# Kernel tuning notes

Measured on AMD Instinct MI355X. Metric: run time of the kernel, lower is better.

The kernel has to match this reference:

```python
import jax, jax.numpy as jnp
import numpy as np
from jax import lax

EPS = 1e-5
SLOPE = 0.01  # default leaky_relu negative slope

def _conv1d(x, w):
    # x: [B, Cin, L], w: [Cout, Cin, K]; padding=1 (same for K=3)
    return lax.conv_general_dilated(x, w, window_strides=(1,), padding=[(1, 1)],
                                    dimension_numbers=('NCH', 'OIH', 'NCH'))

def _bn_train(x, gamma, beta, axes):
    # training-mode BatchNorm: batch stats over `axes`, biased variance
    mean = jnp.mean(x, axis=axes, keepdims=True)
    var = jnp.mean(jnp.square(x - mean), axis=axes, keepdims=True)
    shape = [1] * x.ndim
    shape[1] = x.shape[1]
    g = gamma.reshape(shape); b = beta.reshape(shape)
    return (x - mean) * g / jnp.sqrt(var + EPS) + b

def setup_inputs() -> dict:
    key = jax.random.key(0)
    ks = jax.random.split(key, 6)
    d, d2, out_dim = 64, 128, 128
    bs, T, N = 16, 32, 256
    s = 0.05
    return {
        'x': jax.random.normal(ks[0], (bs, T, N, d), jnp.float32),
        'conv1_w': jax.random.normal(ks[1], (d2, d, 3), jnp.float32) * s,
        'bn1_g': jnp.ones((d2,), jnp.float32), 'bn1_b': jnp.zeros((d2,), jnp.float32),
        'conv2_w': jax.random.normal(ks[2], (d2, d2, 3), jnp.float32) * s,
        'bn2_g': jnp.ones((d2,), jnp.float32), 'bn2_b': jnp.zeros((d2,), jnp.float32),
        'map_w': jax.random.normal(ks[3], (d2, d2), jnp.float32) * s,
        'map_b': jnp.zeros((d2,), jnp.float32),
        'theta_w': jax.random.normal(ks[4], (out_dim, d2), jnp.float32) * s,
        'theta_b': jnp.zeros((out_dim,), jnp.float32),
        'bnS_g': jnp.ones((out_dim,), jnp.float32), 'bnS_b': jnp.zeros((out_dim,), jnp.float32),
    }

def reference(x, conv1_w, bn1_g, bn1_b, conv2_w, bn2_g, bn2_b,
              map_w, map_b, theta_w, theta_b, bnS_g, bnS_b):
    bs, T, N, d = x.shape
    d2 = 2 * d
    # ---- Temporal 1D CNN over time, per node ----
    tem = jnp.transpose(x, (0, 2, 1, 3)).reshape(bs * N, T, d)      # [BN, T, d]
    h = jnp.transpose(tem, (0, 2, 1))                               # [BN, d, T]
    h = jax.nn.relu(_bn_train(_conv1d(h, conv1_w), bn1_g, bn1_b, (0, 2)))
    h = jax.nn.relu(_bn_train(_conv1d(h, conv2_w), bn2_g, bn2_b, (0, 2)))  # [BN, 2d, T]
    # faithful raw reshape (mixes channel/time layout exactly like the torch code)
    tem_out = h.reshape(bs, N, T, d2)
    spa = jnp.transpose(tem_out, (0, 2, 1, 3)).reshape(bs * T, N, d2)  # [B', N, 2d]
    # ---- Dot-product graph construction ----
    mapped = jnp.einsum('bnd,ed->bne', spa, map_w) + map_b            # Linear(2d,2d)
    adj = jnp.einsum('bnd,bmd->bnm', mapped, mapped)                  # [B', N, N]
    eye = jnp.eye(N, dtype=adj.dtype)
    adj = jax.nn.leaky_relu(adj - eye * 1e8, SLOPE)
    adj = jax.nn.softmax(adj, axis=-1) + eye
    # ---- MPNN (k=1): theta(A @ X), BN over channels, leaky_relu ----
    agg = jnp.einsum('bnm,bmd->bnd', adj, spa)                        # bmm(A, X)
    out = jnp.einsum('bnd,od->bno', agg, theta_w) + theta_b           # [B', N, out]
    out = jnp.transpose(out, (0, 2, 1))                               # [B', out, N]
    out = _bn_train(out, bnS_g, bnS_b, (0, 2))
    out = jnp.transpose(out, (0, 2, 1))
    return jax.nn.leaky_relu(out, SLOPE)
```

## Files before the change

kernel.cpp:

```cpp
#include <hip/hip_runtime.h>

#define SLOPE 0.01f
#define EPSB 1e-5f
#define INV_CNT (1.0f/131072.0f)

typedef unsigned short u16;
typedef unsigned int u32;
typedef __attribute__((ext_vector_type(8))) short s16x8;
typedef __attribute__((ext_vector_type(4))) float f4;

__device__ float g_stats[3][2][128];
__device__ float g_sb[3][2][128];
__device__ float g_part[2048][256];
__device__ int   g_cnt[3];
__device__ u16 g_w1h[3][128][64];
__device__ u16 g_w1l[3][128][64];
__device__ u16 g_w2h[3][128][128];
__device__ u16 g_w2l[3][128][128];
__device__ u16 g_wmh[128][128];
__device__ u16 g_wml[128][128];
__device__ u16 g_wqh[128][128];
__device__ u16 g_wql[128][128];
__device__ u16 g_sT[16777216];

__device__ __forceinline__ float lrelu(float x){ return x > 0.f ? x : SLOPE*x; }
__device__ __forceinline__ u16 f2b(float f){
  u32 u = __float_as_uint(f);
  return (u16)((u + 0x7fffu + ((u >> 16) & 1u)) >> 16);
}
__device__ __forceinline__ float b2f(u16 h){ return __uint_as_float(((u32)h) << 16); }
__device__ __forceinline__ u32 pk(float a, float b){ return (u32)f2b(a) | ((u32)f2b(b) << 16); }

__global__ void k_prepw(const float* __restrict__ w1, const float* __restrict__ w2,
                        const float* __restrict__ mapw, const float* __restrict__ thw){
  int idx = blockIdx.x*256 + threadIdx.x;
  if (idx < 768) ((float*)g_stats)[idx] = 0.f;
  if (idx < 3) g_cnt[idx] = 0;
  if (idx < 24576){
    int kk = idx >> 13, r = idx & 8191, co = r >> 6, ci = r & 63;
    float v = w1[co*192 + ci*3 + kk];
    u16 h = f2b(v);
    g_w1h[kk][co][ci] = h; g_w1l[kk][co][ci] = f2b(v - b2f(h));
  } else if (idx < 73728){
    int j = idx - 24576;
    int kk = j >> 14, r = j & 16383, co = r >> 7, ci = r & 127;
    float v = w2[co*384 + ci*3 + kk];
    u16 h = f2b(v);
    g_w2h[kk][co][ci] = h; g_w2l[kk][co][ci] = f2b(v - b2f(h));
  } else if (idx < 90112){
    int j = idx - 73728;
    float v = mapw[j];
    u16 h = f2b(v);
    ((u16*)g_wmh)[j] = h; ((u16*)g_wml)[j] = f2b(v - b2f(h));
  } else if (idx < 106496){
    int j = idx - 90112;
    float v = thw[j];
    u16 h = f2b(v);
    ((u16*)g_wqh)[j] = h; ((u16*)g_wql)[j] = f2b(v - b2f(h));
  }
}

__global__ void k_reduce(const float* __restrict__ g, const float* __restrict__ bta, int which){
  const float* base = &g_part[blockIdx.x*128][0];
  int j = threadIdx.x;
  float s = 0.f;
  #pragma unroll 4
  for (int r = 0; r < 128; ++r) s += base[r*256 + j];
  atomicAdd(&((float*)g_stats)[which*256 + j], s);
  __threadfence();
  __shared__ int lastf;
  __syncthreads();
  if (threadIdx.x == 0) lastf = (atomicAdd(&g_cnt[which], 1) == 15) ? 1 : 0;
  __syncthreads();
  if (lastf){
    __threadfence();
    if (j < 128){
      float sm = atomicAdd(&g_stats[which][0][j], 0.f);
      float sq = atomicAdd(&g_stats[which][1][j], 0.f);
      float mean = sm * INV_CNT;
      float var  = sq * INV_CNT - mean*mean;
      float sc = g[j] * rsqrtf(var + EPSB);
      g_sb[which][0][j] = sc;
      g_sb[which][1][j] = bta[j] - mean*sc;
    }
  }
}

__global__ __launch_bounds__(256, 4) void k_conv1(const float* __restrict__ x, float* __restrict__ y1f){
  __shared__ __align__(16) u16 a0h[2][34][72];
  __shared__ __align__(16) u16 a0l[2][34][72];
  const int bid = blockIdx.x;
  const int bn0 = bid*2;
  const int b = bn0 >> 8, n = bn0 & 255;
  const int tid = threadIdx.x;
  const int w = tid >> 6, l = tid & 63, quad = l >> 4, lm = l & 15;
  f4 acc[2][4];
  #pragma unroll
  for (int i = 0; i < 2; ++i)
    #pragma unroll
    for (int j = 0; j < 4; ++j) acc[i][j] = (f4)0.f;

  {
    int nn = tid >> 7, rem = tid & 127, t = rem >> 2, ci0 = (rem & 3)*16;
    const float* px = x + ((b*32 + t)*256 + n + nn)*64 + ci0;
    u16 hh[16], ll[16];
    #pragma unroll
    for (int j = 0; j < 4; ++j){
      float4 v = *(const float4*)(px + 4*j);
      float vv[4] = {v.x, v.y, v.z, v.w};
      #pragma unroll
      for (int e = 0; e < 4; ++e){
        u16 h = f2b(vv[e]);
        hh[4*j+e] = h; ll[4*j+e] = f2b(vv[e] - b2f(h));
      }
    }
    *(uint4*)&a0h[nn][t+1][ci0]   = *(uint4*)&hh[0];
    *(uint4*)&a0h[nn][t+1][ci0+8] = *(uint4*)&hh[8];
    *(uint4*)&a0l[nn][t+1][ci0]   = *(uint4*)&ll[0];
    *(uint4*)&a0l[nn][t+1][ci0+8] = *(uint4*)&ll[8];
  }
  for (int u = tid; u < 288; u += 256){
    int a = u / 144, rr = u % 144, r = rr / 36, cw = rr % 36;
    u32* base = a ? (u32*)&a0l[r>>1][(r&1)*33][0] : (u32*)&a0h[r>>1][(r&1)*33][0];
    base[cw] = 0u;
  }
  __syncthreads();

  for (int kk = 0; kk < 3; ++kk){
    #pragma unroll
    for (int s = 0; s < 2; ++s){
      int ci0 = s*32 + quad*8;
      s16x8 wh[2], wl[2], bh[4], bl[4];
      #pragma unroll
      for (int i = 0; i < 2; ++i){
        wh[i] = *(const s16x8*)&g_w1h[kk][(2*w+i)*16 + lm][ci0];
        wl[i] = *(const s16x8*)&g_w1l[kk][(2*w+i)*16 + lm][ci0];
      }
      #pragma unroll
      for (int nt = 0; nt < 4; ++nt){
        bh[nt] = *(s16x8*)&a0h[nt>>1][(nt&1)*16 + lm + kk][ci0];
        bl[nt] = *(s16x8*)&a0l[nt>>1][(nt&1)*16 + lm + kk][ci0];
      }
      #pragma unroll
      for (int i = 0; i < 2; ++i)
        #pragma unroll
        for (int nt = 0; nt < 4; ++nt){
          acc[i][nt] = __builtin_amdgcn_mfma_f32_16x16x32_bf16(wh[i], bh[nt], acc[i][nt], 0, 0, 0);
          acc[i][nt] = __builtin_amdgcn_mfma_f32_16x16x32_bf16(wh[i], bl[nt], acc[i][nt], 0, 0, 0);
          acc[i][nt] = __builtin_amdgcn_mfma_f32_16x16x32_bf16(wl[i], bh[nt], acc[i][nt], 0, 0, 0);
        }
    }
  }
  #pragma unroll
  for (int i = 0; i < 2; ++i){
    int co0 = (2*w+i)*16 + quad*4;
    float s0=0,s1=0,s2=0,s3=0,q0=0,q1=0,q2=0,q3=0;
    #pragma unroll
    for (int nt = 0; nt < 4; ++nt){
      f4 a = acc[i][nt];
      int nn = nt >> 1, t = (nt & 1)*16 + lm;
      *(f4*)&y1f[((bn0+nn)*32 + t)*128 + co0] = a;
      s0+=a.x; s1+=a.y; s2+=a.z; s3+=a.w;
      q0+=a.x*a.x; q1+=a.y*a.y; q2+=a.z*a.z; q3+=a.w*a.w;
    }
    #pragma unroll
    for (int m = 1; m < 16; m <<= 1){
      s0+=__shfl_xor(s0,m); s1+=__shfl_xor(s1,m); s2+=__shfl_xor(s2,m); s3+=__shfl_xor(s3,m);
      q0+=__shfl_xor(q0,m); q1+=__shfl_xor(q1,m); q2+=__shfl_xor(q2,m); q3+=__shfl_xor(q3,m);
    }
    if (lm == 0){
      f4 sv = {s0,s1,s2,s3}, qv = {q0,q1,q2,q3};
      *(f4*)&g_part[bid][co0]       = sv;
      *(f4*)&g_part[bid][128 + co0] = qv;
    }
  }
}

__global__ __launch_bounds__(256, 4) void k_conv2(const float* __restrict__ y1f, u16* __restrict__ spa){
  __shared__ __align__(16) u16 a1s[2][34][136];
  const int bid = blockIdx.x;
  const int bn0 = bid*2;
  const int b = bn0 >> 8, n = bn0 & 255;
  const int tid = threadIdx.x;
  const int w = tid >> 6, l = tid & 63, quad = l >> 4, lm = l & 15;
  f4 acc2[4][2];
  #pragma unroll
  for (int mt = 0; mt < 4; ++mt)
    #pragma unroll
    for (int i = 0; i < 2; ++i) acc2[mt][i] = (f4)0.f;

  {
    int nn = tid >> 7, rem = tid & 127, t = rem >> 2, ci0 = (rem & 3)*32;
    const float* py = y1f + ((bn0+nn)*32 + t)*128;
    #pragma unroll
    for (int j = 0; j < 4; ++j){
      float4 v1 = *(const float4*)(py + ci0 + 8*j);
      float4 v2 = *(const float4*)(py + ci0 + 8*j + 4);
      float vv[8] = {v1.x, v1.y, v1.z, v1.w, v2.x, v2.y, v2.z, v2.w};
      u16 oo[8];
      #pragma unroll
      for (int e = 0; e < 8; ++e){
        int ci = ci0 + 8*j + e;
        oo[e] = f2b(fmaxf(fmaf(vv[e], g_sb[0][0][ci], g_sb[0][1][ci]), 0.f));
      }
      *(uint4*)&a1s[nn][t+1][ci0 + 8*j] = *(uint4*)&oo[0];
    }
  }
  for (int u = tid; u < 272; u += 256){
    int r = u/68, cw = u%68;
    ((u32*)&a1s[r>>1][(r&1)*33][0])[cw] = 0u;
  }
  __syncthreads();

  for (int kk = 0; kk < 3; ++kk){
    #pragma unroll
    for (int s = 0; s < 4; ++s){
      int ci0 = s*32 + quad*8;
      s16x8 ax[4], bwh[2], bwl[2];
      #pragma unroll
      for (int i = 0; i < 2; ++i){
        bwh[i] = *(const s16x8*)&g_w2h[kk][(2*w+i)*16 + lm][ci0];
        bwl[i] = *(const s16x8*)&g_w2l[kk][(2*w+i)*16 + lm][ci0];
      }
      #pragma unroll
      for (int mt = 0; mt < 4; ++mt) ax[mt] = *(s16x8*)&a1s[mt>>1][(mt&1)*16 + lm + kk][ci0];
      #pragma unroll
      for (int mt = 0; mt < 4; ++mt)
        #pragma unroll
        for (int i = 0; i < 2; ++i){
          acc2[mt][i] = __builtin_amdgcn_mfma_f32_16x16x32_bf16(ax[mt], bwh[i], acc2[mt][i], 0, 0, 0);
          acc2[mt][i] = __builtin_amdgcn_mfma_f32_16x16x32_bf16(ax[mt], bwl[i], acc2[mt][i], 0, 0, 0);
        }
    }
  }
  #pragma unroll
  for (int i = 0; i < 2; ++i){
    int co = (2*w+i)*16 + lm;
    float s = 0.f, q = 0.f;
    #pragma unroll
    for (int mt = 0; mt < 4; ++mt){
      f4 a = acc2[mt][i];
      int off0 = co*32 + (mt&1)*16 + quad*4;
      int tp = off0 >> 7, cp = off0 & 127;
      int row = (b*32 + tp)*256 + (n + (mt>>1));
      uint2 p; p.x = pk(a.x, a.y); p.y = pk(a.z, a.w);
      *(uint2*)&spa[row*128 + cp] = p;
      s += a.x + a.y + a.z + a.w;
      q += a.x*a.x + a.y*a.y + a.z*a.z + a.w*a.w;
    }
    s += __shfl_xor(s, 16); s += __shfl_xor(s, 32);
    q += __shfl_xor(q, 16); q += __shfl_xor(q, 32);
    if (l < 16){
      g_part[bid][co]       = s;
      g_part[bid][128 + co] = q;
    }
  }
}

__global__ __launch_bounds__(256, 4) void k_gemm128b(const u16* A,
                                                     u16* spaw,
                                                     const float* __restrict__ bvec,
                                                     void* __restrict__ outv,
                                                     int wsel, int do_stats){
  __shared__ __align__(16) u16 As[64][136];
  const u16* Wh = wsel ? &g_wqh[0][0] : &g_wmh[0][0];
  const u16* Wl = wsel ? &g_wql[0][0] : &g_wml[0][0];
  const int bid = blockIdx.x;
  const int rowbase = bid * 64;
  const int tid = threadIdx.x;
  const int w = tid >> 6, l = tid & 63, quad = l >> 4, lm = l & 15;
  f4 acc[2][4];
  #pragma unroll
  for (int i = 0; i < 2; ++i)
    #pragma unroll
    for (int rt = 0; rt < 4; ++rt) acc[i][rt] = (f4)0.f;

  { int r = tid >> 2, c0 = (tid & 3)*32;
    int row = rowbase + r;
    if (wsel == 0){
      int c = ((row >> 8) & 31)*4 + (tid & 3);
      float sc = g_sb[1][0][c], bi = g_sb[1][1][c];
      int mrel = row & 63;
      u16* st = g_sT + (((row >> 6) * 128) << 6);
      #pragma unroll
      for (int j = 0; j < 4; ++j){
        uint4 v = *(const uint4*)&A[row*128 + c0 + 8*j];
        u32 vv[4] = {v.x, v.y, v.z, v.w};
        u16 oo[8];
        #pragma unroll
        for (int e = 0; e < 4; ++e){
          oo[2*e]   = f2b(fmaxf(fmaf(b2f((u16)(vv[e] & 0xffff)), sc, bi), 0.f));
          oo[2*e+1] = f2b(fmaxf(fmaf(b2f((u16)(vv[e] >> 16)),    sc, bi), 0.f));
        }
        uint4 ov = *(uint4*)&oo[0];
        *(uint4*)&As[r][c0 + 8*j] = ov;
        *(uint4*)&spaw[row*128 + c0 + 8*j] = ov;
        #pragma unroll
        for (int e = 0; e < 8; ++e)
          st[(c0 + 8*j + e)*64 + mrel] = oo[e];
      }
    } else {
      #pragma unroll
      for (int j = 0; j < 4; ++j)
        *(uint4*)&As[r][c0 + 8*j] = *(const uint4*)&A[row*128 + c0 + 8*j];
    }
  }
  __syncthreads();

  #pragma unroll
  for (int s = 0; s < 4; ++s){
    int k0 = s*32 + quad*8;
    s16x8 awh[2], awl[2], ba[4];
    #pragma unroll
    for (int i = 0; i < 2; ++i){
      awh[i] = *(const s16x8*)&Wh[((2*w+i)*16 + lm)*128 + k0];
      awl[i] = *(const s16x8*)&Wl[((2*w+i)*16 + lm)*128 + k0];
    }
    #pragma unroll
    for (int rt = 0; rt < 4; ++rt) ba[rt] = *(s16x8*)&As[rt*16 + lm][k0];
    #pragma unroll
    for (int i = 0; i < 2; ++i)
      #pragma unroll
      for (int rt = 0; rt < 4; ++rt){
        acc[i][rt] = __builtin_amdgcn_mfma_f32_16x16x32_bf16(awh[i], ba[rt], acc[i][rt], 0, 0, 0);
        acc[i][rt] = __builtin_amdgcn_mfma_f32_16x16x32_bf16(awl[i], ba[rt], acc[i][rt], 0, 0, 0);
      }
  }
  #pragma unroll
  for (int i = 0; i < 2; ++i){
    int e0 = (2*w+i)*16 + quad*4;
    f4 bv = *(const f4*)&bvec[e0];
    if (wsel == 0){
      u16* mh = (u16*)outv;
      u16* ml = mh + 16777216;
      int dc = e0 >> 5, ec = e0 & 31;
      #pragma unroll
      for (int rt = 0; rt < 4; ++rt){
        int row = rowbase + rt*16 + lm;
        int bp = row >> 8, m = row & 255;
        f4 o = acc[i][rt] + bv;
        float fv[4] = {o.x, o.y, o.z, o.w};
        u16 hh[4], ll[4];
        #pragma unroll
        for (int e = 0; e < 4; ++e){
          u16 h = f2b(fv[e]);
          hh[e] = h; ll[e] = f2b(fv[e] - b2f(h));
        }
        int off = ((bp*4 + dc)*256 + m)*32 + ec;
        *(uint2*)&mh[off] = *(uint2*)&hh[0];
        *(uint2*)&ml[off] = *(uint2*)&ll[0];
      }
    } else {
      float* outp = (float*)outv;
      f4 sv = (f4)0.f, qv = (f4)0.f;
      #pragma unroll
      for (int rt = 0; rt < 4; ++rt){
        int row = rowbase + rt*16 + lm;
        f4 o = acc[i][rt] + bv;
        *(f4*)&outp[row*128 + e0] = o;
        sv += o; qv += o*o;
      }
      if (do_stats){
        #pragma unroll
        for (int m = 1; m < 16; m <<= 1){
          sv.x+=__shfl_xor(sv.x,m); sv.y+=__shfl_xor(sv.y,m); sv.z+=__shfl_xor(sv.z,m); sv.w+=__shfl_xor(sv.w,m);
          qv.x+=__shfl_xor(qv.x,m); qv.y+=__shfl_xor(qv.y,m); qv.z+=__shfl_xor(qv.z,m); qv.w+=__shfl_xor(qv.w,m);
        }
        if (lm == 0){
          *(f4*)&g_part[bid][e0]       = sv;
          *(f4*)&g_part[bid][128 + e0] = qv;
        }
      }
    }
  }
}

__global__ __launch_bounds__(256) void k_adjagg(const u16* __restrict__ mh,
                                                const u16* __restrict__ ml,
                                                const u16* __restrict__ spa,
                                                u16* __restrict__ agg){
  __shared__ __align__(16) char smem[52224];
  u16 (*mbh)[40]   = (u16(*)[40])(smem);
  u16 (*mbl)[40]   = (u16(*)[40])(smem + 20480);
  u16 (*Ps)[264]   = (u16(*)[264])(smem);
  u16 (*spasT)[72] = (u16(*)[72])(smem + 33792);
  const int rb = blockIdx.x;
  const int vb = (rb & 7)*256 + (rb >> 3);
  const int bp = vb >> 2;
  const int nt = vb & 3;
  const int tid = threadIdx.x;
  const int w = tid >> 6, l = tid & 63, quad = l >> 4, lm = l & 15;

  f4 sacc[16];
  #pragma unroll
  for (int ct = 0; ct < 16; ++ct) sacc[ct] = (f4)0.f;

  for (int dc = 0; dc < 4; ++dc){
    __syncthreads();
    {
      const u16* srch = mh + ((bp*4 + dc) << 13);
      const u16* srcl = ml + ((bp*4 + dc) << 13);
      int m0 = tid >> 2, seg = (tid & 3)*8;
      #pragma unroll
      for (int r = 0; r < 4; ++r){
        int m = m0 + r*64;
        *(uint4*)&mbh[m][seg] = *(const uint4*)&srch[m*32 + seg];
        *(uint4*)&mbl[m][seg] = *(const uint4*)&srcl[m*32 + seg];
      }
    }
    __syncthreads();
    s16x8 amh = *(s16x8*)&mbh[nt*64 + w*16 + lm][quad*8];
    s16x8 aml = *(s16x8*)&mbl[nt*64 + w*16 + lm][quad*8];
    #pragma unroll
    for (int ct = 0; ct < 16; ++ct){
      s16x8 bmh = *(s16x8*)&mbh[ct*16 + lm][quad*8];
      s16x8 bml = *(s16x8*)&mbl[ct*16 + lm][quad*8];
      sacc[ct] = __builtin_amdgcn_mfma_f32_16x16x32_bf16(amh, bmh, sacc[ct], 0, 0, 0);
      sacc[ct] = __builtin_amdgcn_mfma_f32_16x16x32_bf16(amh, bml, sacc[ct], 0, 0, 0);
      sacc[ct] = __builtin_amdgcn_mfma_f32_16x16x32_bf16(aml, bmh, sacc[ct], 0, 0, 0);
    }
  }
  __syncthreads();

  #pragma unroll
  for (int r = 0; r < 4; ++r){
    int rowg = nt*64 + w*16 + quad*4 + r;
    float v[16]; float mx = -3.0e38f;
    #pragma unroll
    for (int ct = 0; ct < 16; ++ct){
      float t = sacc[ct][r];
      if (ct*16 + lm == rowg) t -= 1e8f;
      t = lrelu(t);
      v[ct] = t; mx = fmaxf(mx, t);
    }
    #pragma unroll
    for (int m = 1; m < 16; m <<= 1) mx = fmaxf(mx, __shfl_xor(mx, m));
    float sum = 0.f;
    #pragma unroll
    for (int ct = 0; ct < 16; ++ct){ float e = __expf(v[ct] - mx); v[ct] = e; sum += e; }
    #pragma unroll
    for (int m = 1; m < 16; m <<= 1) sum += __shfl_xor(sum, m);
    float inv = 1.0f / sum;
    #pragma unroll
    for (int ct = 0; ct < 16; ++ct)
      Ps[w*16 + quad*4 + r][ct*16 + lm] = f2b(v[ct] * inv);
  }

  f4 acc2[2][4];
  #pragma unroll
  for (int i = 0; i < 2; ++i)
    #pragma unroll
    for (int rt = 0; rt < 4; ++rt) acc2[i][rt] = (f4)0.f;

  for (int mc2 = 0; mc2 < 4; ++mc2){
    __syncthreads();
    {
      const u16* src = g_sT + (((bp*4 + mc2)*128) << 6) + (tid >> 1)*64 + (tid & 1)*32;
      u16* dst = &spasT[tid >> 1][(tid & 1)*32];
      *(uint4*)(dst)      = *(const uint4*)(src);
      *(uint4*)(dst + 8)  = *(const uint4*)(src + 8);
      *(uint4*)(dst + 16) = *(const uint4*)(src + 16);
      *(uint4*)(dst + 24) = *(const uint4*)(src + 24);
    }
    __syncthreads();
    #pragma unroll
    for (int ks = 0; ks < 2; ++ks){
      int m0 = ks*32 + quad*8;
      s16x8 afs[2], bfp[4];
      #pragma unroll
      for (int i = 0; i < 2; ++i) afs[i] = *(s16x8*)&spasT[(2*w+i)*16 + lm][m0];
      #pragma unroll
      for (int rt = 0; rt < 4; ++rt) bfp[rt] = *(s16x8*)&Ps[rt*16 + lm][mc2*64 + m0];
      #pragma unroll
      for (int i = 0; i < 2; ++i)
        #pragma unroll
        for (int rt = 0; rt < 4; ++rt)
          acc2[i][rt] = __builtin_amdgcn_mfma_f32_16x16x32_bf16(afs[i], bfp[rt], acc2[i][rt], 0, 0, 0);
    }
  }
  #pragma unroll
  for (int i = 0; i < 2; ++i){
    int d0 = (2*w+i)*16 + quad*4;
    #pragma unroll
    for (int rt = 0; rt < 4; ++rt){
      int grow = bp*256 + nt*64 + rt*16 + lm;
      uint2 sp = *(const uint2*)&spa[grow*128 + d0];
      f4 a = acc2[i][rt];
      a.x += b2f((u16)(sp.x & 0xffff)); a.y += b2f((u16)(sp.x >> 16));
      a.z += b2f((u16)(sp.y & 0xffff)); a.w += b2f((u16)(sp.y >> 16));
      uint2 p; p.x = pk(a.x, a.y); p.y = pk(a.z, a.w);
      *(uint2*)&agg[grow*128 + d0] = p;
    }
  }
}

__global__ void k_bnout(float* __restrict__ outp){
  int idx = blockIdx.x*256 + threadIdx.x;
  int flat = idx*4;
  int o = flat & 127;
  float4 v = *(const float4*)(outp + flat);
  v.x = lrelu(fmaf(v.x, g_sb[2][0][o+0], g_sb[2][1][o+0]));
  v.y = lrelu(fmaf(v.y, g_sb[2][0][o+1], g_sb[2][1][o+1]));
  v.z = lrelu(fmaf(v.z, g_sb[2][0][o+2], g_sb[2][1][o+2]));
  v.w = lrelu(fmaf(v.w, g_sb[2][0][o+3], g_sb[2][1][o+3]));
  *(float4*)(outp + flat) = v;
}

extern "C" void kernel_launch(void* const* d_in, const int* in_sizes, int n_in,
                              void* d_out, int out_size, void* d_ws, size_t ws_size,
                              hipStream_t stream) {
  const float* x    = (const float*)d_in[0];
  const float* w1   = (const float*)d_in[1];
  const float* bn1g = (const float*)d_in[2];
  const float* bn1b = (const float*)d_in[3];
  const float* w2   = (const float*)d_in[4];
  const float* bn2g = (const float*)d_in[5];
  const float* bn2b = (const float*)d_in[6];
  const float* mapw = (const float*)d_in[7];
  const float* mapb = (const float*)d_in[8];
  const float* thw  = (const float*)d_in[9];
  const float* thb  = (const float*)d_in[10];
  const float* bnSg = (const float*)d_in[11];
  const float* bnSb = (const float*)d_in[12];
  float* outp = (float*)d_out;

  u16* spa = (u16*)d_ws;
  u16* agg = spa + 16777216;

  float* y1f = (float*)d_out;
  u16* mh    = (u16*)d_out;

  k_prepw<<<416, 256, 0, stream>>>(w1, w2, mapw, thw);
  k_conv1<<<2048, 256, 0, stream>>>(x, y1f);
  k_reduce<<<16, 256, 0, stream>>>(bn1g, bn1b, 0);
  k_conv2<<<2048, 256, 0, stream>>>(y1f, spa);
  k_reduce<<<16, 256, 0, stream>>>(bn2g, bn2b, 1);
  k_gemm128b<<<2048, 256, 0, stream>>>(spa, spa, mapb, (void*)mh, 0, 0);
  k_adjagg<<<2048, 256, 0, stream>>>(mh, mh + 16777216, spa, agg);
  k_gemm128b<<<2048, 256, 0, stream>>>(agg, agg, thb, (void*)outp, 1, 1);
  k_reduce<<<16, 256, 0, stream>>>(bnSg, bnSb, 2);
  k_bnout<<<16384, 256, 0, stream>>>(outp);
}
```

Before: 407.5 us.

## Fuse theta GEMM, output BatchNorm and leaky ReLU via grid-wide barrier

```diff
diff --git a/kernel.cpp b/kernel.cpp
--- a/kernel.cpp
+++ b/kernel.cpp
@@ -257,14 +257,13 @@
   }
 }
 
-__global__ __launch_bounds__(256, 4) void k_gemm128b(const u16* A,
-                                                     u16* spaw,
-                                                     const float* __restrict__ bvec,
-                                                     void* __restrict__ outv,
-                                                     int wsel, int do_stats){
+__global__ __launch_bounds__(256, 4) void k_gemm0(const u16* A,
+                                                  u16* spaw,
+                                                  const float* __restrict__ bvec,
+                                                  u16* __restrict__ mh){
   __shared__ __align__(16) u16 As[64][136];
-  const u16* Wh = wsel ? &g_wqh[0][0] : &g_wmh[0][0];
-  const u16* Wl = wsel ? &g_wql[0][0] : &g_wml[0][0];
+  const u16* Wh = &g_wmh[0][0];
+  const u16* Wl = &g_wml[0][0];
   const int bid = blockIdx.x;
   const int rowbase = bid * 64;
   const int tid = threadIdx.x;
@@ -277,32 +276,26 @@
 
   { int r = tid >> 2, c0 = (tid & 3)*32;
     int row = rowbase + r;
-    if (wsel == 0){
-      int c = ((row >> 8) & 31)*4 + (tid & 3);
-      float sc = g_sb[1][0][c], bi = g_sb[1][1][c];
-      int mrel = row & 63;
-      u16* st = g_sT + (((row >> 6) * 128) << 6);
-      #pragma unroll
-      for (int j = 0; j < 4; ++j){
-        uint4 v = *(const uint4*)&A[row*128 + c0 + 8*j];
-        u32 vv[4] = {v.x, v.y, v.z, v.w};
-        u16 oo[8];
-        #pragma unroll
-        for (int e = 0; e < 4; ++e){
-          oo[2*e]   = f2b(fmaxf(fmaf(b2f((u16)(vv[e] & 0xffff)), sc, bi), 0.f));
-          oo[2*e+1] = f2b(fmaxf(fmaf(b2f((u16)(vv[e] >> 16)),    sc, bi), 0.f));
-        }
-        uint4 ov = *(uint4*)&oo[0];
-        *(uint4*)&As[r][c0 + 8*j] = ov;
-        *(uint4*)&spaw[row*128 + c0 + 8*j] = ov;
-        #pragma unroll
-        for (int e = 0; e < 8; ++e)
-          st[(c0 + 8*j + e)*64 + mrel] = oo[e];
-      }
-    } else {
-      #pragma unroll
-      for (int j = 0; j < 4; ++j)
-        *(uint4*)&As[r][c0 + 8*j] = *(const uint4*)&A[row*128 + c0 + 8*j];
+    int c = ((row >> 8) & 31)*4 + (tid & 3);
+    float sc = g_sb[1][0][c], bi = g_sb[1][1][c];
+    int mrel = row & 63;
+    u16* st = g_sT + (((row >> 6) * 128) << 6);
+    #pragma unroll
+    for (int j = 0; j < 4; ++j){
+      uint4 v = *(const uint4*)&A[row*128 + c0 + 8*j];
+      u32 vv[4] = {v.x, v.y, v.z, v.w};
+      u16 oo[8];
+      #pragma unroll
+      for (int e = 0; e < 4; ++e){
+        oo[2*e]   = f2b(fmaxf(fmaf(b2f((u16)(vv[e] & 0xffff)), sc, bi), 0.f));
+        oo[2*e+1] = f2b(fmaxf(fmaf(b2f((u16)(vv[e] >> 16)),    sc, bi), 0.f));
+      }
+      uint4 ov = *(uint4*)&oo[0];
+      *(uint4*)&As[r][c0 + 8*j] = ov;
+      *(uint4*)&spaw[row*128 + c0 + 8*j] = ov;
+      #pragma unroll
+      for (int e = 0; e < 8; ++e)
+        st[(c0 + 8*j + e)*64 + mrel] = oo[e];
     }
   }
   __syncthreads();
@@ -330,47 +323,23 @@
   for (int i = 0; i < 2; ++i){
     int e0 = (2*w+i)*16 + quad*4;
     f4 bv = *(const f4*)&bvec[e0];
-    if (wsel == 0){
-      u16* mh = (u16*)outv;
-      u16* ml = mh + 16777216;
-      int dc = e0 >> 5, ec = e0 & 31;
-      #pragma unroll
-      for (int rt = 0; rt < 4; ++rt){
-        int row = rowbase + rt*16 + lm;
-        int bp = row >> 8, m = row & 255;
-        f4 o = acc[i][rt] + bv;
-        float fv[4] = {o.x, o.y, o.z, o.w};
-        u16 hh[4], ll[4];
-        #pragma unroll
-        for (int e = 0; e < 4; ++e){
-          u16 h = f2b(fv[e]);
-          hh[e] = h; ll[e] = f2b(fv[e] - b2f(h));
-        }
-        int off = ((bp*4 + dc)*256 + m)*32 + ec;
-        *(uint2*)&mh[off] = *(uint2*)&hh[0];
-        *(uint2*)&ml[off] = *(uint2*)&ll[0];
-      }
-    } else {
-      float* outp = (float*)outv;
-      f4 sv = (f4)0.f, qv = (f4)0.f;
-      #pragma unroll
-      for (int rt = 0; rt < 4; ++rt){
-        int row = rowbase + rt*16 + lm;
-        f4 o = acc[i][rt] + bv;
-        *(f4*)&outp[row*128 + e0] = o;
-        sv += o; qv += o*o;
-      }
-      if (do_stats){
-        #pragma unroll
-        for (int m = 1; m < 16; m <<= 1){
-          sv.x+=__shfl_xor(sv.x,m); sv.y+=__shfl_xor(sv.y,m); sv.z+=__shfl_xor(sv.z,m); sv.w+=__shfl_xor(sv.w,m);
-          qv.x+=__shfl_xor(qv.x,m); qv.y+=__shfl_xor(qv.y,m); qv.z+=__shfl_xor(qv.z,m); qv.w+=__shfl_xor(qv.w,m);
-        }
-        if (lm == 0){
-          *(f4*)&g_part[bid][e0]       = sv;
-          *(f4*)&g_part[bid][128 + e0] = qv;
-        }
-      }
+    u16* ml = mh + 16777216;
+    int dc = e0 >> 5, ec = e0 & 31;
+    #pragma unroll
+    for (int rt = 0; rt < 4; ++rt){
+      int row = rowbase + rt*16 + lm;
+      int bp = row >> 8, m = row & 255;
+      f4 o = acc[i][rt] + bv;
+      float fv[4] = {o.x, o.y, o.z, o.w};
+      u16 hh[4], ll[4];
+      #pragma unroll
+      for (int e = 0; e < 4; ++e){
+        u16 h = f2b(fv[e]);
+        hh[e] = h; ll[e] = f2b(fv[e] - b2f(h));
+      }
+      int off = ((bp*4 + dc)*256 + m)*32 + ec;
+      *(uint2*)&mh[off] = *(uint2*)&hh[0];
+      *(uint2*)&ml[off] = *(uint2*)&ll[0];
     }
   }
 }
@@ -494,16 +463,136 @@
   }
 }
 
-__global__ void k_bnout(float* __restrict__ outp){
-  int idx = blockIdx.x*256 + threadIdx.x;
-  int flat = idx*4;
-  int o = flat & 127;
-  float4 v = *(const float4*)(outp + flat);
-  v.x = lrelu(fmaf(v.x, g_sb[2][0][o+0], g_sb[2][1][o+0]));
-  v.y = lrelu(fmaf(v.y, g_sb[2][0][o+1], g_sb[2][1][o+1]));
-  v.z = lrelu(fmaf(v.z, g_sb[2][0][o+2], g_sb[2][1][o+2]));
-  v.w = lrelu(fmaf(v.w, g_sb[2][0][o+3], g_sb[2][1][o+3]));
-  *(float4*)(outp + flat) = v;
+__global__ __launch_bounds__(256, 4) void k_gemm1c(const u16* __restrict__ A,
+                                                   const float* __restrict__ bvec,
+                                                   const float* __restrict__ g,
+                                                   const float* __restrict__ bta,
+                                                   float* __restrict__ outp){
+  __shared__ __align__(16) u16 As[64][136];
+  __shared__ __align__(16) u16 stash[64][132];
+  __shared__ float sbS[2][128];
+  const u16* Wh = &g_wqh[0][0];
+  const u16* Wl = &g_wql[0][0];
+  const int bid = blockIdx.x;
+  const int tid = threadIdx.x;
+  const int w = tid >> 6, l = tid & 63, quad = l >> 4, lm = l & 15;
+
+  f4 o0[2][4], o1[2][4];
+  f4 sv[2] = {(f4)0.f, (f4)0.f}, qv[2] = {(f4)0.f, (f4)0.f};
+
+  #pragma unroll
+  for (int ti = 0; ti < 2; ++ti){
+    const int rowbase = bid*128 + ti*64;
+    f4 acc[2][4];
+    #pragma unroll
+    for (int i = 0; i < 2; ++i)
+      #pragma unroll
+      for (int rt = 0; rt < 4; ++rt) acc[i][rt] = (f4)0.f;
+
+    if (ti) __syncthreads();
+    { int r = tid >> 2, c0 = (tid & 3)*32;
+      #pragma unroll
+      for (int j = 0; j < 4; ++j)
+        *(uint4*)&As[r][c0 + 8*j] = *(const uint4*)&A[(rowbase + r)*128 + c0 + 8*j];
+    }
+    __syncthreads();
+
+    #pragma unroll
+    for (int s = 0; s < 4; ++s){
+      int k0 = s*32 + quad*8;
+      s16x8 awh[2], awl[2], ba[4];
+      #pragma unroll
+      for (int i = 0; i < 2; ++i){
+        awh[i] = *(const s16x8*)&Wh[((2*w+i)*16 + lm)*128 + k0];
+        awl[i] = *(const s16x8*)&Wl[((2*w+i)*16 + lm)*128 + k0];
+      }
+      #pragma unroll
+      for (int rt = 0; rt < 4; ++rt) ba[rt] = *(s16x8*)&As[rt*16 + lm][k0];
+      #pragma unroll
+      for (int i = 0; i < 2; ++i)
+        #pragma unroll
+        for (int rt = 0; rt < 4; ++rt){
+          acc[i][rt] = __builtin_amdgcn_mfma_f32_16x16x32_bf16(awh[i], ba[rt], acc[i][rt], 0, 0, 0);
+          acc[i][rt] = __builtin_amdgcn_mfma_f32_16x16x32_bf16(awl[i], ba[rt], acc[i][rt], 0, 0, 0);
+        }
+    }
+    #pragma unroll
+    for (int i = 0; i < 2; ++i){
+      int e0 = (2*w+i)*16 + quad*4;
+      f4 bv = *(const f4*)&bvec[e0];
+      #pragma unroll
+      for (int rt = 0; rt < 4; ++rt){
+        f4 o = acc[i][rt] + bv;
+        if (ti == 0){
+          o0[i][rt] = o;
+          uint2 p; p.x = pk(o.x, o.y); p.y = pk(o.z, o.w);
+          *(uint2*)&stash[rt*16 + lm][e0] = p;
+        } else {
+          o1[i][rt] = o;
+        }
+        sv[i] += o; qv[i] += o*o;
+      }
+    }
+  }
+  (void)o0;
+
+  #pragma unroll
+  for (int i = 0; i < 2; ++i){
+    #pragma unroll
+    for (int m = 1; m < 16; m <<= 1){
+      sv[i].x+=__shfl_xor(sv[i].x,m); sv[i].y+=__shfl_xor(sv[i].y,m);
+      sv[i].z+=__shfl_xor(sv[i].z,m); sv[i].w+=__shfl_xor(sv[i].w,m);
+      qv[i].x+=__shfl_xor(qv[i].x,m); qv[i].y+=__shfl_xor(qv[i].y,m);
+      qv[i].z+=__shfl_xor(qv[i].z,m); qv[i].w+=__shfl_xor(qv[i].w,m);
+    }
+    if (lm == 0){
+      int e0 = (2*w+i)*16 + quad*4;
+      atomicAdd(&g_stats[2][0][e0+0], sv[i].x); atomicAdd(&g_stats[2][0][e0+1], sv[i].y);
+      atomicAdd(&g_stats[2][0][e0+2], sv[i].z); atomicAdd(&g_stats[2][0][e0+3], sv[i].w);
+      atomicAdd(&g_stats[2][1][e0+0], qv[i].x); atomicAdd(&g_stats[2][1][e0+1], qv[i].y);
+      atomicAdd(&g_stats[2][1][e0+2], qv[i].z); atomicAdd(&g_stats[2][1][e0+3], qv[i].w);
+    }
+  }
+  __threadfence();
+  __syncthreads();
+  if (tid == 0){
+    atomicAdd(&g_cnt[2], 1);
+    while (atomicAdd(&g_cnt[2], 0) < 1024) __builtin_amdgcn_s_sleep(16);
+  }
+  __syncthreads();
+  __threadfence();
+  if (tid < 128){
+    float sm = atomicAdd(&g_stats[2][0][tid], 0.f);
+    float sq = atomicAdd(&g_stats[2][1][tid], 0.f);
+    float mean = sm * INV_CNT;
+    float var  = sq * INV_CNT - mean*mean;
+    float sc = g[tid] * rsqrtf(var + EPSB);
+    sbS[0][tid] = sc;
+    sbS[1][tid] = bta[tid] - mean*sc;
+  }
+  __syncthreads();
+  #pragma unroll
+  for (int i = 0; i < 2; ++i){
+    int e0 = (2*w+i)*16 + quad*4;
+    f4 sc = *(const f4*)&sbS[0][e0];
+    f4 bi = *(const f4*)&sbS[1][e0];
+    #pragma unroll
+    for (int rt = 0; rt < 4; ++rt){
+      uint2 p = *(const uint2*)&stash[rt*16 + lm][e0];
+      f4 t0;
+      t0.x = b2f((u16)(p.x & 0xffff)); t0.y = b2f((u16)(p.x >> 16));
+      t0.z = b2f((u16)(p.y & 0xffff)); t0.w = b2f((u16)(p.y >> 16));
+      f4 r0;
+      r0.x = lrelu(fmaf(t0.x, sc.x, bi.x)); r0.y = lrelu(fmaf(t0.y, sc.y, bi.y));
+      r0.z = lrelu(fmaf(t0.z, sc.z, bi.z)); r0.w = lrelu(fmaf(t0.w, sc.w, bi.w));
+      *(f4*)&outp[(bid*128 + rt*16 + lm)*128 + e0] = r0;
+      f4 o = o1[i][rt];
+      f4 r1;
+      r1.x = lrelu(fmaf(o.x, sc.x, bi.x)); r1.y = lrelu(fmaf(o.y, sc.y, bi.y));
+      r1.z = lrelu(fmaf(o.z, sc.z, bi.z)); r1.w = lrelu(fmaf(o.w, sc.w, bi.w));
+      *(f4*)&outp[(bid*128 + 64 + rt*16 + lm)*128 + e0] = r1;
+    }
+  }
 }
 
 extern "C" void kernel_launch(void* const* d_in, const int* in_sizes, int n_in,
@@ -535,9 +624,7 @@
   k_reduce<<<16, 256, 0, stream>>>(bn1g, bn1b, 0);
   k_conv2<<<2048, 256, 0, stream>>>(y1f, spa);
   k_reduce<<<16, 256, 0, stream>>>(bn2g, bn2b, 1);
-  k_gemm128b<<<2048, 256, 0, stream>>>(spa, spa, mapb, (void*)mh, 0, 0);
+  k_gemm0<<<2048, 256, 0, stream>>>(spa, spa, mapb, mh);
   k_adjagg<<<2048, 256, 0, stream>>>(mh, mh + 16777216, spa, agg);
-  k_gemm128b<<<2048, 256, 0, stream>>>(agg, agg, thb, (void*)outp, 1, 1);
-  k_reduce<<<16, 256, 0, stream>>>(bnSg, bnSb, 2);
-  k_bnout<<<16384, 256, 0, stream>>>(outp);
-}
+  k_gemm1c<<<1024, 256, 0, stream>>>(agg, thb, bnSg, bnSb, outp);
+}
```

Measured after the change: 692.3 us. +69.9%, slower.

## Store intermediates in bf16 and drop the transposed spa copy

Applied to the files above, without the earlier changes.

```diff
diff --git a/kernel.cpp b/kernel.cpp
--- a/kernel.cpp
+++ b/kernel.cpp
@@ -21,7 +21,6 @@
 __device__ u16 g_wml[128][128];
 __device__ u16 g_wqh[128][128];
 __device__ u16 g_wql[128][128];
-__device__ u16 g_sT[16777216];
 
 __device__ __forceinline__ float lrelu(float x){ return x > 0.f ? x : SLOPE*x; }
 __device__ __forceinline__ u16 f2b(float f){
@@ -86,7 +85,7 @@
   }
 }
 
-__global__ __launch_bounds__(256, 4) void k_conv1(const float* __restrict__ x, float* __restrict__ y1f){
+__global__ __launch_bounds__(256, 4) void k_conv1(const float* __restrict__ x, u16* __restrict__ y1b){
   __shared__ __align__(16) u16 a0h[2][34][72];
   __shared__ __align__(16) u16 a0l[2][34][72];
   const int bid = blockIdx.x;
@@ -159,7 +158,8 @@
     for (int nt = 0; nt < 4; ++nt){
       f4 a = acc[i][nt];
       int nn = nt >> 1, t = (nt & 1)*16 + lm;
-      *(f4*)&y1f[((bn0+nn)*32 + t)*128 + co0] = a;
+      uint2 p; p.x = pk(a.x, a.y); p.y = pk(a.z, a.w);
+      *(uint2*)&y1b[((bn0+nn)*32 + t)*128 + co0] = p;
       s0+=a.x; s1+=a.y; s2+=a.z; s3+=a.w;
       q0+=a.x*a.x; q1+=a.y*a.y; q2+=a.z*a.z; q3+=a.w*a.w;
     }
@@ -176,7 +176,7 @@
   }
 }
 
-__global__ __launch_bounds__(256, 4) void k_conv2(const float* __restrict__ y1f, u16* __restrict__ spa){
+__global__ __launch_bounds__(256, 4) void k_conv2(const u16* __restrict__ y1b, u16* __restrict__ spa){
   __shared__ __align__(16) u16 a1s[2][34][136];
   const int bid = blockIdx.x;
   const int bn0 = bid*2;
@@ -191,17 +191,17 @@
 
   {
     int nn = tid >> 7, rem = tid & 127, t = rem >> 2, ci0 = (rem & 3)*32;
-    const float* py = y1f + ((bn0+nn)*32 + t)*128;
+    const u16* py = y1b + ((bn0+nn)*32 + t)*128;
     #pragma unroll
     for (int j = 0; j < 4; ++j){
-      float4 v1 = *(const float4*)(py + ci0 + 8*j);
-      float4 v2 = *(const float4*)(py + ci0 + 8*j + 4);
-      float vv[8] = {v1.x, v1.y, v1.z, v1.w, v2.x, v2.y, v2.z, v2.w};
+      uint4 v = *(const uint4*)(py + ci0 + 8*j);
+      u32 vv[4] = {v.x, v.y, v.z, v.w};
       u16 oo[8];
       #pragma unroll
-      for (int e = 0; e < 8; ++e){
-        int ci = ci0 + 8*j + e;
-        oo[e] = f2b(fmaxf(fmaf(vv[e], g_sb[0][0][ci], g_sb[0][1][ci]), 0.f));
+      for (int e = 0; e < 4; ++e){
+        int ci = ci0 + 8*j + 2*e;
+        oo[2*e]   = f2b(fmaxf(fmaf(b2f((u16)(vv[e] & 0xffff)), g_sb[0][0][ci],   g_sb[0][1][ci]),   0.f));
+        oo[2*e+1] = f2b(fmaxf(fmaf(b2f((u16)(vv[e] >> 16)),    g_sb[0][0][ci+1], g_sb[0][1][ci+1]), 0.f));
       }
       *(uint4*)&a1s[nn][t+1][ci0 + 8*j] = *(uint4*)&oo[0];
     }
@@ -257,14 +257,13 @@
   }
 }
 
-__global__ __launch_bounds__(256, 4) void k_gemm128b(const u16* A,
-                                                     u16* spaw,
-                                                     const float* __restrict__ bvec,
-                                                     void* __restrict__ outv,
-                                                     int wsel, int do_stats){
+__global__ __launch_bounds__(256, 4) void k_gemm0(const u16* A,
+                                                  u16* spaw,
+                                                  const float* __restrict__ bvec,
+                                                  u16* __restrict__ mh){
   __shared__ __align__(16) u16 As[64][136];
-  const u16* Wh = wsel ? &g_wqh[0][0] : &g_wmh[0][0];
-  const u16* Wl = wsel ? &g_wql[0][0] : &g_wml[0][0];
+  const u16* Wh = &g_wmh[0][0];
+  const u16* Wl = &g_wml[0][0];
   const int bid = blockIdx.x;
   const int rowbase = bid * 64;
   const int tid = threadIdx.x;
@@ -277,32 +276,21 @@
 
   { int r = tid >> 2, c0 = (tid & 3)*32;
     int row = rowbase + r;
-    if (wsel == 0){
-      int c = ((row >> 8) & 31)*4 + (tid & 3);
-      float sc = g_sb[1][0][c], bi = g_sb[1][1][c];
-      int mrel = row & 63;
-      u16* st = g_sT + (((row >> 6) * 128) << 6);
-      #pragma unroll
-      for (int j = 0; j < 4; ++j){
-        uint4 v = *(const uint4*)&A[row*128 + c0 + 8*j];
-        u32 vv[4] = {v.x, v.y, v.z, v.w};
-        u16 oo[8];
-        #pragma unroll
-        for (int e = 0; e < 4; ++e){
-          oo[2*e]   = f2b(fmaxf(fmaf(b2f((u16)(vv[e] & 0xffff)), sc, bi), 0.f));
-          oo[2*e+1] = f2b(fmaxf(fmaf(b2f((u16)(vv[e] >> 16)),    sc, bi), 0.f));
-        }
-        uint4 ov = *(uint4*)&oo[0];
-        *(uint4*)&As[r][c0 + 8*j] = ov;
-        *(uint4*)&spaw[row*128 + c0 + 8*j] = ov;
-        #pragma unroll
-        for (int e = 0; e < 8; ++e)
-          st[(c0 + 8*j + e)*64 + mrel] = oo[e];
-      }
-    } else {
-      #pragma unroll
-      for (int j = 0; j < 4; ++j)
-        *(uint4*)&As[r][c0 + 8*j] = *(const uint4*)&A[row*128 + c0 + 8*j];
+    int c = ((row >> 8) & 31)*4 + (tid & 3);
+    float sc = g_sb[1][0][c], bi = g_sb[1][1][c];
+    #pragma unroll
+    for (int j = 0; j < 4; ++j){
+      uint4 v = *(const uint4*)&A[row*128 + c0 + 8*j];
+      u32 vv[4] = {v.x, v.y, v.z, v.w};
+      u16 oo[8];
+      #pragma unroll
+      for (int e = 0; e < 4; ++e){
+        oo[2*e]   = f2b(fmaxf(fmaf(b2f((u16)(vv[e] & 0xffff)), sc, bi), 0.f));
+        oo[2*e+1] = f2b(fmaxf(fmaf(b2f((u16)(vv[e] >> 16)),    sc, bi), 0.f));
+      }
+      uint4 ov = *(uint4*)&oo[0];
+      *(uint4*)&As[r][c0 + 8*j] = ov;
+      *(uint4*)&spaw[row*128 + c0 + 8*j] = ov;
     }
   }
   __syncthreads();
@@ -330,47 +318,23 @@
   for (int i = 0; i < 2; ++i){
     int e0 = (2*w+i)*16 + quad*4;
     f4 bv = *(const f4*)&bvec[e0];
-    if (wsel == 0){
-      u16* mh = (u16*)outv;
-      u16* ml = mh + 16777216;
-      int dc = e0 >> 5, ec = e0 & 31;
-      #pragma unroll
-      for (int rt = 0; rt < 4; ++rt){
-        int row = rowbase + rt*16 + lm;
-        int bp = row >> 8, m = row & 255;
-        f4 o = acc[i][rt] + bv;
-        float fv[4] = {o.x, o.y, o.z, o.w};
-        u16 hh[4], ll[4];
-        #pragma unroll
-        for (int e = 0; e < 4; ++e){
-          u16 h = f2b(fv[e]);
-          hh[e] = h; ll[e] = f2b(fv[e] - b2f(h));
-        }
-        int off = ((bp*4 + dc)*256 + m)*32 + ec;
-        *(uint2*)&mh[off] = *(uint2*)&hh[0];
-        *(uint2*)&ml[off] = *(uint2*)&ll[0];
-      }
-    } else {
-      float* outp = (float*)outv;
-      f4 sv = (f4)0.f, qv = (f4)0.f;
-      #pragma unroll
-      for (int rt = 0; rt < 4; ++rt){
-        int row = rowbase + rt*16 + lm;
-        f4 o = acc[i][rt] + bv;
-        *(f4*)&outp[row*128 + e0] = o;
-        sv += o; qv += o*o;
-      }
-      if (do_stats){
-        #pragma unroll
-        for (int m = 1; m < 16; m <<= 1){
-          sv.x+=__shfl_xor(sv.x,m); sv.y+=__shfl_xor(sv.y,m); sv.z+=__shfl_xor(sv.z,m); sv.w+=__shfl_xor(sv.w,m);
-          qv.x+=__shfl_xor(qv.x,m); qv.y+=__shfl_xor(qv.y,m); qv.z+=__shfl_xor(qv.z,m); qv.w+=__shfl_xor(qv.w,m);
-        }
-        if (lm == 0){
-          *(f4*)&g_part[bid][e0]       = sv;
-          *(f4*)&g_part[bid][128 + e0] = qv;
-        }
-      }
+    u16* ml = mh + 16777216;
+    int dc = e0 >> 5, ec = e0 & 31;
+    #pragma unroll
+    for (int rt = 0; rt < 4; ++rt){
+      int row = rowbase + rt*16 + lm;
+      int bp = row >> 8, m = row & 255;
+      f4 o = acc[i][rt] + bv;
+      float fv[4] = {o.x, o.y, o.z, o.w};
+      u16 hh[4], ll[4];
+      #pragma unroll
+      for (int e = 0; e < 4; ++e){
+        u16 h = f2b(fv[e]);
+        hh[e] = h; ll[e] = f2b(fv[e] - b2f(h));
+      }
+      int off = ((bp*4 + dc)*256 + m)*32 + ec;
+      *(uint2*)&mh[off] = *(uint2*)&hh[0];
+      *(uint2*)&ml[off] = *(uint2*)&ll[0];
     }
   }
 }
@@ -455,12 +419,17 @@
   for (int mc2 = 0; mc2 < 4; ++mc2){
     __syncthreads();
     {
-      const u16* src = g_sT + (((bp*4 + mc2)*128) << 6) + (tid >> 1)*64 + (tid & 1)*32;
-      u16* dst = &spasT[tid >> 1][(tid & 1)*32];
-      *(uint4*)(dst)      = *(const uint4*)(src);
-      *(uint4*)(dst + 8)  = *(const uint4*)(src + 8);
-      *(uint4*)(dst + 16) = *(const uint4*)(src + 16);
-      *(uint4*)(dst + 24) = *(const uint4*)(src + 24);
+      int mlo = tid & 63;
+      int db = (tid >> 6)*8;
+      const u16* ps = spa + (bp*256 + mc2*64 + mlo)*128;
+      #pragma unroll
+      for (int r = 0; r < 4; ++r){
+        int d0 = db + r*32;
+        uint4 v = *(const uint4*)(ps + d0);
+        u16 h[8]; *(uint4*)&h[0] = v;
+        #pragma unroll
+        for (int j = 0; j < 8; ++j) spasT[d0+j][mlo] = h[j];
+      }
     }
     __syncthreads();
     #pragma unroll
@@ -494,16 +463,90 @@
   }
 }
 
-__global__ void k_bnout(float* __restrict__ outp){
+__global__ __launch_bounds__(256, 4) void k_gemm1(const u16* __restrict__ A,
+                                                  const float* __restrict__ bvec,
+                                                  u16* __restrict__ outpre){
+  __shared__ __align__(16) u16 As[64][136];
+  const u16* Wh = &g_wqh[0][0];
+  const u16* Wl = &g_wql[0][0];
+  const int bid = blockIdx.x;
+  const int rowbase = bid * 64;
+  const int tid = threadIdx.x;
+  const int w = tid >> 6, l = tid & 63, quad = l >> 4, lm = l & 15;
+  f4 acc[2][4];
+  #pragma unroll
+  for (int i = 0; i < 2; ++i)
+    #pragma unroll
+    for (int rt = 0; rt < 4; ++rt) acc[i][rt] = (f4)0.f;
+
+  { int r = tid >> 2, c0 = (tid & 3)*32;
+    #pragma unroll
+    for (int j = 0; j < 4; ++j)
+      *(uint4*)&As[r][c0 + 8*j] = *(const uint4*)&A[(rowbase + r)*128 + c0 + 8*j];
+  }
+  __syncthreads();
+
+  #pragma unroll
+  for (int s = 0; s < 4; ++s){
+    int k0 = s*32 + quad*8;
+    s16x8 awh[2], awl[2], ba[4];
+    #pragma unroll
+    for (int i = 0; i < 2; ++i){
+      awh[i] = *(const s16x8*)&Wh[((2*w+i)*16 + lm)*128 + k0];
+      awl[i] = *(const s16x8*)&Wl[((2*w+i)*16 + lm)*128 + k0];
+    }
+    #pragma unroll
+    for (int rt = 0; rt < 4; ++rt) ba[rt] = *(s16x8*)&As[rt*16 + lm][k0];
+    #pragma unroll
+    for (int i = 0; i < 2; ++i)
+      #pragma unroll
+      for (int rt = 0; rt < 4; ++rt){
+        acc[i][rt] = __builtin_amdgcn_mfma_f32_16x16x32_bf16(awh[i], ba[rt], acc[i][rt], 0, 0, 0);
+        acc[i][rt] = __builtin_amdgcn_mfma_f32_16x16x32_bf16(awl[i], ba[rt], acc[i][rt], 0, 0, 0);
+      }
+  }
+  #pragma unroll
+  for (int i = 0; i < 2; ++i){
+    int e0 = (2*w+i)*16 + quad*4;
+    f4 bv = *(const f4*)&bvec[e0];
+    f4 sv = (f4)0.f, qv = (f4)0.f;
+    #pragma unroll
+    for (int rt = 0; rt < 4; ++rt){
+      int row = rowbase + rt*16 + lm;
+      f4 o = acc[i][rt] + bv;
+      uint2 p; p.x = pk(o.x, o.y); p.y = pk(o.z, o.w);
+      *(uint2*)&outpre[row*128 + e0] = p;
+      sv += o; qv += o*o;
+    }
+    #pragma unroll
+    for (int m = 1; m < 16; m <<= 1){
+      sv.x+=__shfl_xor(sv.x,m); sv.y+=__shfl_xor(sv.y,m); sv.z+=__shfl_xor(sv.z,m); sv.w+=__shfl_xor(sv.w,m);
+      qv.x+=__shfl_xor(qv.x,m); qv.y+=__shfl_xor(qv.y,m); qv.z+=__shfl_xor(qv.z,m); qv.w+=__shfl_xor(qv.w,m);
+    }
+    if (lm == 0){
+      *(f4*)&g_part[bid][e0]       = sv;
+      *(f4*)&g_part[bid][128 + e0] = qv;
+    }
+  }
+}
+
+__global__ void k_bnout(const u16* __restrict__ outpre, float* __restrict__ outp){
   int idx = blockIdx.x*256 + threadIdx.x;
-  int flat = idx*4;
+  int flat = idx*8;
   int o = flat & 127;
-  float4 v = *(const float4*)(outp + flat);
-  v.x = lrelu(fmaf(v.x, g_sb[2][0][o+0], g_sb[2][1][o+0]));
-  v.y = lrelu(fmaf(v.y, g_sb[2][0][o+1], g_sb[2][1][o+1]));
-  v.z = lrelu(fmaf(v.z, g_sb[2][0][o+2], g_sb[2][1][o+2]));
-  v.w = lrelu(fmaf(v.w, g_sb[2][0][o+3], g_sb[2][1][o+3]));
-  *(float4*)(outp + flat) = v;
+  uint4 v = *(const uint4*)(outpre + flat);
+  u32 vv[4] = {v.x, v.y, v.z, v.w};
+  float4 r0, r1;
+  float rr[8];
+  #pragma unroll
+  for (int e = 0; e < 4; ++e){
+    rr[2*e]   = lrelu(fmaf(b2f((u16)(vv[e] & 0xffff)), g_sb[2][0][o+2*e],   g_sb[2][1][o+2*e]));
+    rr[2*e+1] = lrelu(fmaf(b2f((u16)(vv[e] >> 16)),    g_sb[2][0][o+2*e+1], g_sb[2][1][o+2*e+1]));
+  }
+  r0.x = rr[0]; r0.y = rr[1]; r0.z = rr[2]; r0.w = rr[3];
+  r1.x = rr[4]; r1.y = rr[5]; r1.z = rr[6]; r1.w = rr[7];
+  *(float4*)(outp + flat)     = r0;
+  *(float4*)(outp + flat + 4) = r1;
 }
 
 extern "C" void kernel_launch(void* const* d_in, const int* in_sizes, int n_in,
@@ -524,20 +567,21 @@
   const float* bnSb = (const float*)d_in[12];
   float* outp = (float*)d_out;
 
-  u16* spa = (u16*)d_ws;
-  u16* agg = spa + 16777216;
-
-  float* y1f = (float*)d_out;
-  u16* mh    = (u16*)d_out;
+  u16* spa    = (u16*)d_ws;
+  u16* agg    = spa + 16777216;
+  u16* outpre = spa;
+
+  u16* y1b = (u16*)d_out;
+  u16* mh  = (u16*)d_out;
 
   k_prepw<<<416, 256, 0, stream>>>(w1, w2, mapw, thw);
-  k_conv1<<<2048, 256, 0, stream>>>(x, y1f);
+  k_conv1<<<2048, 256, 0, stream>>>(x, y1b);
   k_reduce<<<16, 256, 0, stream>>>(bn1g, bn1b, 0);
-  k_conv2<<<2048, 256, 0, stream>>>(y1f, spa);
+  k_conv2<<<2048, 256, 0, stream>>>(y1b, spa);
   k_reduce<<<16, 256, 0, stream>>>(bn2g, bn2b, 1);
-  k_gemm128b<<<2048, 256, 0, stream>>>(spa, spa, mapb, (void*)mh, 0, 0);
+  k_gemm0<<<2048, 256, 0, stream>>>(spa, spa, mapb, mh);
   k_adjagg<<<2048, 256, 0, stream>>>(mh, mh + 16777216, spa, agg);
-  k_gemm128b<<<2048, 256, 0, stream>>>(agg, agg, thb, (void*)outp, 1, 1);
+  k_gemm1<<<2048, 256, 0, stream>>>(agg, thb, outpre);
   k_reduce<<<16, 256, 0, stream>>>(bnSg, bnSb, 2);
-  k_bnout<<<16384, 256, 0, stream>>>(outp);
-}
+  k_bnout<<<8192, 256, 0, stream>>>(outpre, outp);
+}
```

After: 393.6 us. 3.4% less time.
